# Performance work log

Measured on AMD Instinct MI355X. Metric: run time of the kernel, lower is better.

## Reference

```python
import jax, jax.numpy as jnp
import numpy as np

B, S, E = 2, 2048, 1024
H = 32
DK = E // H  # 32, must equal H for the bilinear einsum to type-check
FFN = 4096
EPS = 1e-5


def layer_norm(x, g, b):
    m = jnp.mean(x, axis=-1, keepdims=True)
    v = jnp.mean((x - m) ** 2, axis=-1, keepdims=True)
    return (x - m) * jax.lax.rsqrt(v + EPS) * g + b


def setup_inputs() -> dict:
    key = jax.random.key(0)
    ks = jax.random.split(key, 16)
    sc = lambda fan_in: 1.0 / np.sqrt(fan_in)
    return {
        "x": jax.random.normal(ks[0], (B, S, E), jnp.float32),
        "Wq": jax.random.normal(ks[1], (E, E), jnp.float32) * sc(E),
        "bq": jax.random.normal(ks[2], (E,), jnp.float32) * 0.02,
        "Wk": jax.random.normal(ks[3], (E, E), jnp.float32) * sc(E),
        "bk": jax.random.normal(ks[4], (E,), jnp.float32) * 0.02,
        "Wv": jax.random.normal(ks[5], (E, E), jnp.float32) * sc(E),
        "bv": jax.random.normal(ks[6], (E,), jnp.float32) * 0.02,
        "kernelW": jax.random.normal(ks[7], (DK, H), jnp.float32),
        "Wo": jax.random.normal(ks[8], (E, E), jnp.float32) * sc(E),
        "bo": jax.random.normal(ks[9], (E,), jnp.float32) * 0.02,
        "W1": jax.random.normal(ks[10], (E, FFN), jnp.float32) * sc(E),
        "b1": jax.random.normal(ks[11], (FFN,), jnp.float32) * 0.02,
        "W2": jax.random.normal(ks[12], (FFN, E), jnp.float32) * sc(FFN),
        "b2": jax.random.normal(ks[13], (E,), jnp.float32) * 0.02,
        "g1": jnp.ones((E,), jnp.float32),
        "beta1": jnp.zeros((E,), jnp.float32),
        "g2": jnp.ones((E,), jnp.float32),
        "beta2": jnp.zeros((E,), jnp.float32),
    }


def reference(x, Wq, bq, Wk, bk, Wv, bv, kernelW, Wo, bo, W1, b1, W2, b2, g1, beta1, g2, beta2):
    # projections -> [B, H, S, DK]
    split = lambda t: t.reshape(B, S, H, DK).transpose(0, 2, 1, 3)
    q = split(x @ Wq + bq)
    k = split(x @ Wk + bk)
    v = split(x @ Wv + bv)
    # bilinear quantum-kernel score: sim[b,h,i,j] = sum_d q[b,h,i,d]*W[d,h]*k[b,h,j,d]
    sim = jnp.einsum('bhqd,dh,bhkd->bhqk', q, kernelW, k)
    attn = jax.nn.softmax(sim, axis=-1)  # dropout is identity at eval
    out = jnp.matmul(attn, v)  # [B, H, S, DK]
    out = out.transpose(0, 2, 1, 3).reshape(B, S, E) @ Wo + bo
    x = layer_norm(x + out, g1, beta1)
    ffn = jax.nn.relu(x @ W1 + b1) @ W2 + b2
    return layer_norm(x + ffn, g2, beta2)
```

## Files before the change

kernel.cpp:

```cpp
#include <hip/hip_runtime.h>


typedef unsigned short u16;
typedef unsigned int u32;
typedef __bf16 bf16x8 __attribute__((ext_vector_type(8)));
typedef float f32x4 __attribute__((ext_vector_type(4)));
typedef float f32x16 __attribute__((ext_vector_type(16)));

__device__ __forceinline__ u16 f2b(float f) {
  union { float f; unsigned u; } x; x.f = f;
  unsigned r = x.u + 0x7FFFu + ((x.u >> 16) & 1u);
  return (u16)(r >> 16);
}

__device__ __forceinline__ unsigned pkbf(float lo, float hi) {
  unsigned r;
  asm("v_cvt_pk_bf16_f32 %0, %1, %2" : "=v"(r) : "v"(lo), "v"(hi));
  return r;
}

__device__ __forceinline__ float expo2(float x) {
#if __has_builtin(__builtin_amdgcn_exp2f)
  return __builtin_amdgcn_exp2f(x);
#else
  return exp2f(x);
#endif
}

#define GLDS16(gp, lp)                                                         \
  __builtin_amdgcn_global_load_lds(                                            \
      (const __attribute__((address_space(1))) void*)(gp),                     \
      (__attribute__((address_space(3))) void*)(lp), 16, 0, 0)

__global__ __launch_bounds__(256) void transpose_cast(
    const float* __restrict__ W, u16* __restrict__ WT, int K, int N) {
  __shared__ float tile[32][33];
  const int tx = threadIdx.x & 31, ty = threadIdx.x >> 5;
  const int n0 = blockIdx.x * 32, k0 = blockIdx.y * 32;
#pragma unroll
  for (int i = 0; i < 4; ++i)
    tile[ty + 8 * i][tx] = W[(size_t)(k0 + ty + 8 * i) * N + n0 + tx];
  __syncthreads();
#pragma unroll
  for (int i = 0; i < 4; ++i)
    WT[(size_t)(n0 + ty + 8 * i) * K + k0 + tx] = f2b(tile[tx][ty + 8 * i]);
}

__global__ __launch_bounds__(256) void cast_b(const float* __restrict__ x,
                                              u16* __restrict__ y) {
  int i = blockIdx.x * 256 + threadIdx.x;
  float4 v = ((const float4*)x)[i];
  ushort4 o;
  o.x = f2b(v.x); o.y = f2b(v.y); o.z = f2b(v.z); o.w = f2b(v.w);
  ((ushort4*)y)[i] = o;
}

template <int MODE, int BN>
__global__ __launch_bounds__(256) void gemmT(
    const u16* __restrict__ A, const u16* __restrict__ BT,
    const float* __restrict__ bias, const float* __restrict__ bias2,
    const float* __restrict__ bias3, const float* __restrict__ res,
    void* __restrict__ outp, const float* __restrict__ kW, int N_, int K_) {
  constexpr int ABYT = 128 * 32 * 2;
  constexpr int BBYT = BN * 32 * 2;
  constexpr int STRIDE = ABYT + BBYT;
  constexpr int MI = (BN == 128) ? 4 : 2;
  __shared__ __align__(16) char SH[2 * STRIDE];
  const int t = threadIdx.x, lane = t & 63, wid = t >> 6;
  const int m0 = blockIdx.y * 128, n0 = blockIdx.x * BN;
  const int wr = (BN == 128) ? (wid >> 1) * 64 : wid * 32;
  const int wc = (BN == 128) ? (wid & 1) * 64 : 0;
  const int lr = lane & 15, lg = lane >> 4;
  const int K = K_;

  f32x4 acc[MI][4] = {};

  const u16* ga0 = A + (size_t)(m0 + (t >> 2)) * K + (t & 3) * 8;
  const u16* ga1 = ga0 + (size_t)64 * K;
  const u16* gb0 = BT + (size_t)(n0 + (t >> 2)) * K + (t & 3) * 8;
  const u16* gb1 = gb0 + (size_t)64 * K;
  const int stA = wid * 1024;

#define STAGE(CUR, KT)                                                         \
  {                                                                            \
    char* l_ = (char*)SH + (CUR) * STRIDE + stA;                               \
    const size_t o_ = (size_t)(KT) * 32;                                       \
    GLDS16(ga0 + o_, l_);                                                      \
    GLDS16(ga1 + o_, l_ + 4096);                                               \
    GLDS16(gb0 + o_, l_ + ABYT);                                               \
    if constexpr (BN == 128) GLDS16(gb1 + o_, l_ + ABYT + 4096);               \
  }

  const int nk = K >> 5;
  STAGE(0, 0);
  __syncthreads();
  int cur = 0;
  for (int kt = 0; kt < nk; ++kt) {
    if (kt + 1 < nk) STAGE(cur ^ 1, kt + 1);
    const char* l = (const char*)SH + cur * STRIDE;
    bf16x8 af[MI], bf[4];
#pragma unroll
    for (int i = 0; i < MI; ++i)
      af[i] = *(const bf16x8*)(l + (wr + i * 16 + lr) * 64 + lg * 16);
#pragma unroll
    for (int i = 0; i < 4; ++i)
      bf[i] = *(const bf16x8*)(l + ABYT + (wc + i * 16 + lr) * 64 + lg * 16);
#pragma unroll
    for (int mi = 0; mi < MI; ++mi)
#pragma unroll
      for (int ni = 0; ni < 4; ++ni)
        acc[mi][ni] = __builtin_amdgcn_mfma_f32_16x16x32_bf16(
            af[mi], bf[ni], acc[mi][ni], 0, 0, 0);
    __syncthreads();
    cur ^= 1;
  }
#undef STAGE

#pragma unroll
  for (int mi = 0; mi < MI; ++mi) {
#pragma unroll
    for (int ni = 0; ni < 4; ++ni) {
      const int row = m0 + wr + mi * 16 + lg * 4;
      const int col = n0 + wc + ni * 16 + lr;
      f32x4 v = acc[mi][ni];
      if constexpr (MODE == 2) {
        const float bv = bias[col];
        float* o = (float*)outp;
#pragma unroll
        for (int r = 0; r < 4; ++r) {
          const int rr = row + r;
          o[(size_t)rr * N_ + col] = v[r] + bv + res[(size_t)rr * N_ + col];
        }
      } else if constexpr (MODE == 3) {
        const float bv = bias[col];
        u16* o = (u16*)outp;
#pragma unroll
        for (int r = 0; r < 4; ++r) {
          const int rr = row + r;
          float y = v[r] + bv;
          o[(size_t)rr * N_ + col] = f2b(y > 0.f ? y : 0.f);
        }
      } else {
        const int proj = col >> 10, c = col & 1023;
        const int h = c >> 5, d = c & 31;
        u16* qout = (u16*)outp;
        if (proj == 0) {
          const float bv = bias[c];
          const float sc = kW[d * 32 + h] * 1.44269504089f;
#pragma unroll
          for (int r = 0; r < 4; ++r) {
            const int rr = row + r;
            const int bb = rr >> 11, s = rr & 2047;
            qout[(size_t)(((bb * 32 + h) * 2048) + s) * 32 + d] =
                f2b((v[r] + bv) * sc);
          }
        } else if (proj == 1) {
          const float bv = bias2[c];
          u16* kout = qout + 4194304;
          const int c2 = d >> 3;
#pragma unroll
          for (int r = 0; r < 4; ++r) {
            const int rr = row + r;
            const int bb = rr >> 11, s = rr & 2047;
            const int k = s & 63;
            const int g = ((k >> 5) << 1) | (c2 >> 1);
            kout[(size_t)(bb * 32 + h) * 65536 + (s >> 6) * 2048 + g * 512 +
                 (c2 & 1) * 256 + (k & 31) * 8 + (d & 7)] = f2b(v[r] + bv);
          }
        } else {
          const float bv = bias3[c];
          u16* vout = qout + 8388608;
          const int bb = row >> 11, s0 = row & 2047;
          const int k = s0 & 63;
          const int cc = k >> 3, rb = cc >> 1, hb = cc & 1, e = k & 7;
          ushort4 st;
          st.x = f2b(v[0] + bv); st.y = f2b(v[1] + bv);
          st.z = f2b(v[2] + bv); st.w = f2b(v[3] + bv);
          *(ushort4*)(vout + (size_t)(bb * 32 + h) * 65536 +
                      (s0 >> 6) * 2048 + rb * 512 + hb * 256 + d * 8 + e) = st;
        }
      }
    }
  }
}

__device__ __forceinline__ void attn_tile(
    const bf16x8& k0, const bf16x8& k1, const bf16x8& k2, const bf16x8& k3,
    const bf16x8& v0, const bf16x8& v1, const bf16x8& v2, const bf16x8& v3,
    const bf16x8& qb0, const bf16x8& qb1,
    f32x16& acc, float& la, float& lb, float& lc, float& ld) {
  const f32x16 z16 = {};
  f32x16 s0 = __builtin_amdgcn_mfma_f32_32x32x16_bf16(k0, qb0, z16, 0, 0, 0);
  s0 = __builtin_amdgcn_mfma_f32_32x32x16_bf16(k1, qb1, s0, 0, 0, 0);
  f32x16 s1 = __builtin_amdgcn_mfma_f32_32x32x16_bf16(k2, qb0, z16, 0, 0, 0);
  s1 = __builtin_amdgcn_mfma_f32_32x32x16_bf16(k3, qb1, s1, 0, 0, 0);
  float p0[16], p1[16];
#pragma unroll
  for (int r = 0; r < 16; ++r) p0[r] = expo2(s0[r]);
#pragma unroll
  for (int r = 0; r < 16; ++r) p1[r] = expo2(s1[r]);
#pragma unroll
  for (int r = 0; r < 4; ++r) {
    la += p0[r] + p1[r];
    lb += p0[4 + r] + p1[4 + r];
    lc += p0[8 + r] + p1[8 + r];
    ld += p0[12 + r] + p1[12 + r];
  }
  {
    u32 x0 = pkbf(p0[0], p0[1]), x1 = pkbf(p0[2], p0[3]);
    u32 y0 = pkbf(p0[4], p0[5]), y1 = pkbf(p0[6], p0[7]);
    asm("v_permlane32_swap_b32 %0, %1" : "+v"(x0), "+v"(y0));
    asm("v_permlane32_swap_b32 %0, %1" : "+v"(x1), "+v"(y1));
    union { u32 d[4]; bf16x8 v; } u;
    u.d[0] = x0; u.d[1] = x1; u.d[2] = y0; u.d[3] = y1;
    acc = __builtin_amdgcn_mfma_f32_32x32x16_bf16(v0, u.v, acc, 0, 0, 0);
  }
  {
    u32 x0 = pkbf(p0[8], p0[9]), x1 = pkbf(p0[10], p0[11]);
    u32 y0 = pkbf(p0[12], p0[13]), y1 = pkbf(p0[14], p0[15]);
    asm("v_permlane32_swap_b32 %0, %1" : "+v"(x0), "+v"(y0));
    asm("v_permlane32_swap_b32 %0, %1" : "+v"(x1), "+v"(y1));
    union { u32 d[4]; bf16x8 v; } u;
    u.d[0] = x0; u.d[1] = x1; u.d[2] = y0; u.d[3] = y1;
    acc = __builtin_amdgcn_mfma_f32_32x32x16_bf16(v1, u.v, acc, 0, 0, 0);
  }
  {
    u32 x0 = pkbf(p1[0], p1[1]), x1 = pkbf(p1[2], p1[3]);
    u32 y0 = pkbf(p1[4], p1[5]), y1 = pkbf(p1[6], p1[7]);
    asm("v_permlane32_swap_b32 %0, %1" : "+v"(x0), "+v"(y0));
    asm("v_permlane32_swap_b32 %0, %1" : "+v"(x1), "+v"(y1));
    union { u32 d[4]; bf16x8 v; } u;
    u.d[0] = x0; u.d[1] = x1; u.d[2] = y0; u.d[3] = y1;
    acc = __builtin_amdgcn_mfma_f32_32x32x16_bf16(v2, u.v, acc, 0, 0, 0);
  }
  {
    u32 x0 = pkbf(p1[8], p1[9]), x1 = pkbf(p1[10], p1[11]);
    u32 y0 = pkbf(p1[12], p1[13]), y1 = pkbf(p1[14], p1[15]);
    asm("v_permlane32_swap_b32 %0, %1" : "+v"(x0), "+v"(y0));
    asm("v_permlane32_swap_b32 %0, %1" : "+v"(x1), "+v"(y1));
    union { u32 d[4]; bf16x8 v; } u;
    u.d[0] = x0; u.d[1] = x1; u.d[2] = y0; u.d[3] = y1;
    acc = __builtin_amdgcn_mfma_f32_32x32x16_bf16(v3, u.v, acc, 0, 0, 0);
  }
}

__global__ __launch_bounds__(256) void attn_kernel(
    const u16* __restrict__ Q, const u16* __restrict__ K,
    const u16* __restrict__ VT, u16* __restrict__ O) {
  __shared__ __align__(16) char LDSB[32768];
  const int t = threadIdx.x, wid = t >> 6, lane = t & 63;
  const int qg = wid & 1, kh = wid >> 1;
  const int bid = blockIdx.x;
  const int swz = (bid & 7) * 256 + (bid >> 3);
  const int bh = swz >> 5;
  const int qt = swz & 31;
  const int q0 = qt * 64 + qg * 32;
  const int lq = lane & 31, hi = lane >> 5;
  const u16* Qh = Q + (size_t)bh * 65536;
  const u16* Kh = K + (size_t)bh * 65536;
  const u16* Vh = VT + (size_t)bh * 65536;

  const bf16x8 qb0 = *(const bf16x8*)(Qh + (size_t)(q0 + lq) * 32 + hi * 8);
  const bf16x8 qb1 = *(const bf16x8*)(Qh + (size_t)(q0 + lq) * 32 + 16 + hi * 8);

  const u16* kg = Kh + wid * 512 + lane * 8;
  const u16* vg = Vh + wid * 512 + lane * 8;
  const int lds_w = wid * 1024;

#define STAGEA(CUR, I)                                                         \
  {                                                                            \
    char* b_ = LDSB + (CUR) * 16384 + lds_w;                                   \
    GLDS16(kg + (size_t)(I) * 2048, b_);                                       \
    GLDS16(vg + (size_t)(I) * 2048, b_ + 4096);                                \
    GLDS16(kg + (size_t)(16 + (I)) * 2048, b_ + 8192);                         \
    GLDS16(vg + (size_t)(16 + (I)) * 2048, b_ + 12288);                        \
  }

  f32x16 acc = {};
  float la = 0.f, lb = 0.f, lc = 0.f, ld = 0.f;

  STAGEA(0, 0);
  __syncthreads();
  int cur = 0;
#pragma unroll 1
  for (int i = 0; i < 16; ++i) {
    if (i < 15) STAGEA(cur ^ 1, i + 1);
    const char* kb = LDSB + cur * 16384 + kh * 8192 + lane * 16;
    const bf16x8 ka0 = *(const bf16x8*)(kb);
    const bf16x8 ka1 = *(const bf16x8*)(kb + 1024);
    const bf16x8 ka2 = *(const bf16x8*)(kb + 2048);
    const bf16x8 ka3 = *(const bf16x8*)(kb + 3072);
    const bf16x8 va0 = *(const bf16x8*)(kb + 4096);
    const bf16x8 va1 = *(const bf16x8*)(kb + 5120);
    const bf16x8 va2 = *(const bf16x8*)(kb + 6144);
    const bf16x8 va3 = *(const bf16x8*)(kb + 7168);
    attn_tile(ka0, ka1, ka2, ka3, va0, va1, va2, va3, qb0, qb1,
              acc, la, lb, lc, ld);
    __syncthreads();
    cur ^= 1;
  }
#undef STAGEA

  float lrun = (la + lb) + (lc + ld);
  lrun += __shfl_xor(lrun, 32);

  float* sm_acc = (float*)LDSB;
  float* sm_l = (float*)(LDSB + 8192);
  if (kh == 1) {
    sm_l[qg * 32 + lq] = lrun;
#pragma unroll
    for (int r = 0; r < 16; ++r) sm_acc[(qg * 64 + lane) * 16 + r] = acc[r];
  }
  __syncthreads();
  if (kh == 0) {
    const float inv = 1.f / (lrun + sm_l[qg * 32 + lq]);
    const int bb = bh >> 5, h = bh & 31;
    u16* o = O + (size_t)(bb * 2048 + q0 + lq) * 1024 + h * 32;
#pragma unroll
    for (int g = 0; g < 4; ++g) {
      ushort4 st;
      st.x = f2b((acc[g * 4 + 0] + sm_acc[(qg * 64 + lane) * 16 + g * 4 + 0]) * inv);
      st.y = f2b((acc[g * 4 + 1] + sm_acc[(qg * 64 + lane) * 16 + g * 4 + 1]) * inv);
      st.z = f2b((acc[g * 4 + 2] + sm_acc[(qg * 64 + lane) * 16 + g * 4 + 2]) * inv);
      st.w = f2b((acc[g * 4 + 3] + sm_acc[(qg * 64 + lane) * 16 + g * 4 + 3]) * inv);
      *(ushort4*)(o + g * 8 + hi * 4) = st;
    }
  }
}

template <int WB>
__global__ __launch_bounds__(256) void ln_kernel(
    const float* X, const float* __restrict__ g, const float* __restrict__ b,
    float* outf, u16* __restrict__ outb) {
  const int wid = threadIdx.x >> 6, lane = threadIdx.x & 63;
  const int row = blockIdx.x * 4 + wid;
  const float4* X4 = (const float4*)(X + (size_t)row * 1024);
  float4 xs[4];
  float s = 0.f, sq = 0.f;
#pragma unroll
  for (int i = 0; i < 4; ++i) {
    xs[i] = X4[lane + i * 64];
    s += xs[i].x + xs[i].y + xs[i].z + xs[i].w;
    sq += xs[i].x * xs[i].x + xs[i].y * xs[i].y + xs[i].z * xs[i].z + xs[i].w * xs[i].w;
  }
#pragma unroll
  for (int m = 1; m < 64; m <<= 1) { s += __shfl_xor(s, m); sq += __shfl_xor(sq, m); }
  const float mean = s * (1.f / 1024.f);
  float var = sq * (1.f / 1024.f) - mean * mean;
  var = var > 0.f ? var : 0.f;
  const float rstd = rsqrtf(var + 1e-5f);
  const float4* g4 = (const float4*)g;
  const float4* b4 = (const float4*)b;
  float4* of = (float4*)(outf + (size_t)row * 1024);
#pragma unroll
  for (int i = 0; i < 4; ++i) {
    const int c = lane + i * 64;
    const float4 gv = g4[c], bv = b4[c], x = xs[i];
    float4 y;
    y.x = (x.x - mean) * rstd * gv.x + bv.x;
    y.y = (x.y - mean) * rstd * gv.y + bv.y;
    y.z = (x.z - mean) * rstd * gv.z + bv.z;
    y.w = (x.w - mean) * rstd * gv.w + bv.w;
    of[c] = y;
    if constexpr (WB) {
      ushort4 yb;
      yb.x = f2b(y.x); yb.y = f2b(y.y); yb.z = f2b(y.z); yb.w = f2b(y.w);
      ((ushort4*)(outb + (size_t)row * 1024))[c] = yb;
    }
  }
}

extern "C" void kernel_launch(void* const* d_in, const int* in_sizes, int n_in,
                              void* d_out, int out_size, void* d_ws,
                              size_t ws_size, hipStream_t stream) {
  const float* x   = (const float*)d_in[0];
  const float* Wq  = (const float*)d_in[1];
  const float* bq  = (const float*)d_in[2];
  const float* Wk  = (const float*)d_in[3];
  const float* bk  = (const float*)d_in[4];
  const float* Wv  = (const float*)d_in[5];
  const float* bv  = (const float*)d_in[6];
  const float* kW  = (const float*)d_in[7];
  const float* Wo  = (const float*)d_in[8];
  const float* bo  = (const float*)d_in[9];
  const float* W1  = (const float*)d_in[10];
  const float* b1  = (const float*)d_in[11];
  const float* W2  = (const float*)d_in[12];
  const float* b2  = (const float*)d_in[13];
  const float* g1  = (const float*)d_in[14];
  const float* be1 = (const float*)d_in[15];
  const float* g2  = (const float*)d_in[16];
  const float* be2 = (const float*)d_in[17];

  char* ws = (char*)d_ws;
  const size_t MB = 1024 * 1024;
  u16*   WqT = (u16*)(ws + 0 * MB);
  u16*   WkT = (u16*)(ws + 2 * MB);
  u16*   WvT = (u16*)(ws + 4 * MB);
  u16*   WoT = (u16*)(ws + 6 * MB);
  u16*   W1T = (u16*)(ws + 8 * MB);
  u16*   W2T = (u16*)(ws + 16 * MB);
  float* r1  = (float*)(ws + 24 * MB);
  u16*   xb  = (u16*)(ws + 40 * MB);
  u16*   qhB = (u16*)(ws + 48 * MB);
  u16*   khB = (u16*)(ws + 56 * MB);
  u16*   vTB = (u16*)(ws + 64 * MB);
  u16*   hf  = (u16*)(ws + 40 * MB);
  u16*   ao  = (u16*)(ws + 72 * MB);
  u16*   x1b = (u16*)(ws + 80 * MB);
  float* r2  = (float*)(ws + 72 * MB);

  const dim3 blk(256);

  transpose_cast<<<dim3(32, 32), blk, 0, stream>>>(Wq, WqT, 1024, 1024);
  transpose_cast<<<dim3(32, 32), blk, 0, stream>>>(Wk, WkT, 1024, 1024);
  transpose_cast<<<dim3(32, 32), blk, 0, stream>>>(Wv, WvT, 1024, 1024);
  transpose_cast<<<dim3(32, 32), blk, 0, stream>>>(Wo, WoT, 1024, 1024);
  transpose_cast<<<dim3(128, 32), blk, 0, stream>>>(W1, W1T, 1024, 4096);
  transpose_cast<<<dim3(32, 128), blk, 0, stream>>>(W2, W2T, 4096, 1024);
  cast_b<<<4096, blk, 0, stream>>>(x, xb);

  gemmT<5, 128><<<dim3(24, 32), blk, 0, stream>>>(
      xb, WqT, bq, bk, bv, nullptr, qhB, kW, 3072, 1024);

  attn_kernel<<<2048, blk, 0, stream>>>(qhB, khB, vTB, ao);

  gemmT<2, 64><<<dim3(16, 32), blk, 0, stream>>>(
      ao, WoT, bo, nullptr, nullptr, x, r1, nullptr, 1024, 1024);
  ln_kernel<1><<<1024, blk, 0, stream>>>(r1, g1, be1, r1, x1b);
  gemmT<3, 128><<<dim3(32, 32), blk, 0, stream>>>(
      x1b, W1T, b1, nullptr, nullptr, nullptr, hf, nullptr, 4096, 1024);
  gemmT<2, 64><<<dim3(16, 32), blk, 0, stream>>>(
      hf, W2T, b2, nullptr, nullptr, r1, r2, nullptr, 1024, 4096);
  ln_kernel<0><<<1024, blk, 0, stream>>>(r2, g2, be2, (float*)d_out, nullptr);

  (void)in_sizes; (void)n_in; (void)out_size; (void)ws_size;
}
```

Before: 272.9 us.

## Split-K the FFN down-projection and fuse partial sum into final layernorm

Splits the K=4096 W2 GEMM into two halves launched as separate blocks (1024 blocks instead of 512) that write fp32 partials to two buffers. A new layernorm kernel sums the partials, residual and bias before normalizing. It also adds a grouped block-index swizzle to all GEMM launches for better L2 locality. The cost is extra fp32 partial traffic and a workspace reuse of the weight region for one partial.

After: 270.5 us. Within noise of the previous version (-0.9%).

```diff
diff --git a/kernel.cpp b/kernel.cpp
--- a/kernel.cpp
+++ b/kernel.cpp
@@ -67,17 +67,26 @@
   constexpr int MI = (BN == 128) ? 4 : 2;
   __shared__ __align__(16) char SH[2 * STRIDE];
   const int t = threadIdx.x, lane = t & 63, wid = t >> 6;
-  const int m0 = blockIdx.y * 128, n0 = blockIdx.x * BN;
+  const int gx = gridDim.x;
+  const int id = blockIdx.y * gx + blockIdx.x;
+  const int nb = gx * gridDim.y;
+  const int sid = (id & 7) * (nb >> 3) + (id >> 3);
+  const int bx = sid % gx;
+  int by = sid / gx;
+  int kh6 = 0;
+  if constexpr (MODE == 6) { kh6 = by >> 5; by &= 31; }
+  const int m0 = by * 128, n0 = bx * BN;
   const int wr = (BN == 128) ? (wid >> 1) * 64 : wid * 32;
   const int wc = (BN == 128) ? (wid & 1) * 64 : 0;
   const int lr = lane & 15, lg = lane >> 4;
   const int K = K_;
+  const int koff = (MODE == 6) ? kh6 * 2048 : 0;
 
   f32x4 acc[MI][4] = {};
 
-  const u16* ga0 = A + (size_t)(m0 + (t >> 2)) * K + (t & 3) * 8;
+  const u16* ga0 = A + (size_t)(m0 + (t >> 2)) * K + koff + (t & 3) * 8;
   const u16* ga1 = ga0 + (size_t)64 * K;
-  const u16* gb0 = BT + (size_t)(n0 + (t >> 2)) * K + (t & 3) * 8;
+  const u16* gb0 = BT + (size_t)(n0 + (t >> 2)) * K + koff + (t & 3) * 8;
   const u16* gb1 = gb0 + (size_t)64 * K;
   const int stA = wid * 1024;
 
@@ -91,7 +100,7 @@
     if constexpr (BN == 128) GLDS16(gb1 + o_, l_ + ABYT + 4096);               \
   }
 
-  const int nk = K >> 5;
+  const int nk = (MODE == 6) ? 64 : (K >> 5);
   STAGE(0, 0);
   __syncthreads();
   int cur = 0;
@@ -139,6 +148,13 @@
           const int rr = row + r;
           float y = v[r] + bv;
           o[(size_t)rr * N_ + col] = f2b(y > 0.f ? y : 0.f);
+        }
+      } else if constexpr (MODE == 6) {
+        float* o = (kh6 == 0) ? (float*)outp : (float*)res;
+#pragma unroll
+        for (int r = 0; r < 4; ++r) {
+          const int rr = row + r;
+          o[(size_t)rr * N_ + col] = v[r];
         }
       } else {
         const int proj = col >> 10, c = col & 1023;
@@ -370,6 +386,54 @@
   }
 }
 
+__global__ __launch_bounds__(256) void ln2sum_kernel(
+    const float* __restrict__ PA, const float* __restrict__ PB,
+    const float* __restrict__ R, const float* __restrict__ bias,
+    const float* __restrict__ g, const float* __restrict__ b,
+    float* __restrict__ out) {
+  const int wid = threadIdx.x >> 6, lane = threadIdx.x & 63;
+  const int row = blockIdx.x * 4 + wid;
+  const float4* A4 = (const float4*)(PA + (size_t)row * 1024);
+  const float4* B4 = (const float4*)(PB + (size_t)row * 1024);
+  const float4* R4 = (const float4*)(R + (size_t)row * 1024);
+  const float4* Bi4 = (const float4*)bias;
+  float4 xs[4];
+  float s = 0.f, sq = 0.f;
+#pragma unroll
+  for (int i = 0; i < 4; ++i) {
+    const int c = lane + i * 64;
+    const float4 a = A4[c], pb = B4[c], r = R4[c], bi = Bi4[c];
+    float4 x;
+    x.x = a.x + pb.x + r.x + bi.x;
+    x.y = a.y + pb.y + r.y + bi.y;
+    x.z = a.z + pb.z + r.z + bi.z;
+    x.w = a.w + pb.w + r.w + bi.w;
+    xs[i] = x;
+    s += x.x + x.y + x.z + x.w;
+    sq += x.x * x.x + x.y * x.y + x.z * x.z + x.w * x.w;
+  }
+#pragma unroll
+  for (int m = 1; m < 64; m <<= 1) { s += __shfl_xor(s, m); sq += __shfl_xor(sq, m); }
+  const float mean = s * (1.f / 1024.f);
+  float var = sq * (1.f / 1024.f) - mean * mean;
+  var = var > 0.f ? var : 0.f;
+  const float rstd = rsqrtf(var + 1e-5f);
+  const float4* g4 = (const float4*)g;
+  const float4* b4 = (const float4*)b;
+  float4* of = (float4*)(out + (size_t)row * 1024);
+#pragma unroll
+  for (int i = 0; i < 4; ++i) {
+    const int c = lane + i * 64;
+    const float4 gv = g4[c], bv = b4[c], x = xs[i];
+    float4 y;
+    y.x = (x.x - mean) * rstd * gv.x + bv.x;
+    y.y = (x.y - mean) * rstd * gv.y + bv.y;
+    y.z = (x.z - mean) * rstd * gv.z + bv.z;
+    y.w = (x.w - mean) * rstd * gv.w + bv.w;
+    of[c] = y;
+  }
+}
+
 extern "C" void kernel_launch(void* const* d_in, const int* in_sizes, int n_in,
                               void* d_out, int out_size, void* d_ws,
                               size_t ws_size, hipStream_t stream) {
@@ -395,8 +459,6 @@
   char* ws = (char*)d_ws;
   const size_t MB = 1024 * 1024;
   u16*   WqT = (u16*)(ws + 0 * MB);
-  u16*   WkT = (u16*)(ws + 2 * MB);
-  u16*   WvT = (u16*)(ws + 4 * MB);
   u16*   WoT = (u16*)(ws + 6 * MB);
   u16*   W1T = (u16*)(ws + 8 * MB);
   u16*   W2T = (u16*)(ws + 16 * MB);
@@ -408,13 +470,14 @@
   u16*   hf  = (u16*)(ws + 40 * MB);
   u16*   ao  = (u16*)(ws + 72 * MB);
   u16*   x1b = (u16*)(ws + 80 * MB);
-  float* r2  = (float*)(ws + 72 * MB);
+  float* r2a = (float*)(ws + 0 * MB);
+  float* r2b = (float*)(ws + 72 * MB);
 
   const dim3 blk(256);
 
   transpose_cast<<<dim3(32, 32), blk, 0, stream>>>(Wq, WqT, 1024, 1024);
-  transpose_cast<<<dim3(32, 32), blk, 0, stream>>>(Wk, WkT, 1024, 1024);
-  transpose_cast<<<dim3(32, 32), blk, 0, stream>>>(Wv, WvT, 1024, 1024);
+  transpose_cast<<<dim3(32, 32), blk, 0, stream>>>(Wk, WqT + 1048576, 1024, 1024);
+  transpose_cast<<<dim3(32, 32), blk, 0, stream>>>(Wv, WqT + 2097152, 1024, 1024);
   transpose_cast<<<dim3(32, 32), blk, 0, stream>>>(Wo, WoT, 1024, 1024);
   transpose_cast<<<dim3(128, 32), blk, 0, stream>>>(W1, W1T, 1024, 4096);
   transpose_cast<<<dim3(32, 128), blk, 0, stream>>>(W2, W2T, 4096, 1024);
@@ -430,9 +493,10 @@
   ln_kernel<1><<<1024, blk, 0, stream>>>(r1, g1, be1, r1, x1b);
   gemmT<3, 128><<<dim3(32, 32), blk, 0, stream>>>(
       x1b, W1T, b1, nullptr, nullptr, nullptr, hf, nullptr, 4096, 1024);
-  gemmT<2, 64><<<dim3(16, 32), blk, 0, stream>>>(
-      hf, W2T, b2, nullptr, nullptr, r1, r2, nullptr, 1024, 4096);
-  ln_kernel<0><<<1024, blk, 0, stream>>>(r2, g2, be2, (float*)d_out, nullptr);
+  gemmT<6, 64><<<dim3(16, 64), blk, 0, stream>>>(
+      hf, W2T, nullptr, nullptr, nullptr, r2b, r2a, nullptr, 1024, 4096);
+  ln2sum_kernel<<<1024, blk, 0, stream>>>(r2a, r2b, r1, b2, g2, be2,
+                                          (float*)d_out);
 
   (void)in_sizes; (void)n_in; (void)out_size; (void)ws_size;
 }
```
